# Performance work log

Measured on AMD Instinct MI355X. Metric: run time of the kernel, lower is better.

## Reference

```python
import jax, jax.numpy as jnp
import numpy as np

N, E = 50000, 800000
IN_FEATS, H, F = 128, 2, 64
NEG_SLOPE = 0.2


def _gat_conv(x, W, attn_l, attn_r, bias, src, dst):
    """DGL-style GATConv. x:[N,IN], W:[H*F,IN], attn_l/attn_r:[H,F], bias:[H*F]. Returns [N,H,F]."""
    z = (x @ W.T).reshape(N, H, F)                      # node projections
    el = jnp.einsum('nhf,hf->nh', z, attn_l)            # [N,H]
    er = jnp.einsum('nhf,hf->nh', z, attn_r)            # [N,H]
    e = jax.nn.leaky_relu(el[src] + er[dst], NEG_SLOPE) # [E,H] edge logits
    # edge softmax over incoming edges of each destination node
    m = jax.ops.segment_max(e, dst, num_segments=N)     # [N,H]
    ex = jnp.exp(e - m[dst])
    s = jax.ops.segment_sum(ex, dst, num_segments=N)    # [N,H]
    alpha = ex / s[dst]                                 # [E,H]
    msg = alpha[:, :, None] * z[src]                    # [E,H,F]
    out = jax.ops.segment_sum(msg, dst, num_segments=N) # [N,H,F]
    return out + bias.reshape(1, H, F)


def setup_inputs() -> dict:
    key = jax.random.key(0)
    ks = jax.random.split(key, 10)
    x = jax.random.normal(ks[0], (N, IN_FEATS), dtype=jnp.float32)
    h = jax.random.normal(ks[1], (N, H, F), dtype=jnp.float32)
    src = jax.random.randint(ks[2], (E,), 0, N, dtype=jnp.int32)
    dst = jax.random.randint(ks[3], (E,), 0, N, dtype=jnp.int32)
    sc = 1.0 / np.sqrt(IN_FEATS)
    W = jax.random.normal(ks[4], (3, H * F, IN_FEATS), dtype=jnp.float32) * sc  # r,u,c fc weights
    attn_l = jax.random.normal(ks[5], (3, H, F), dtype=jnp.float32) * 0.1
    attn_r = jax.random.normal(ks[6], (3, H, F), dtype=jnp.float32) * 0.1
    conv_bias = jax.random.normal(ks[7], (3, H * F), dtype=jnp.float32) * 0.02
    gate_bias = jax.random.uniform(ks[8], (3, H, F), dtype=jnp.float32)  # torch.rand init
    return {"x": x, "h": h, "W": W, "attn_l": attn_l, "attn_r": attn_r,
            "conv_bias": conv_bias, "gate_bias": gate_bias, "src": src, "dst": dst}


def reference(x, h, W, attn_l, attn_r, conv_bias, gate_bias, src, dst):
    # r, u, c gates; each GATConv is applied to x (use_hidden=False branch)
    r = jax.nn.sigmoid(_gat_conv(x, W[0], attn_l[0], attn_r[0], conv_bias[0], src, dst) + gate_bias[0])
    u = jax.nn.sigmoid(_gat_conv(x, W[1], attn_l[1], attn_r[1], conv_bias[1], src, dst) + gate_bias[1])
    # note: original computes h_ = r*h but never uses it in this branch (dead code)
    c = jax.nn.sigmoid(_gat_conv(x, W[2], attn_l[2], attn_r[2], conv_bias[2], src, dst) + gate_bias[2])
    new_h = u * h + (1.0 - u) * c
    return new_h
```

## Files before the change

### kernel.cpp

```cpp
#include <hip/hip_runtime.h>
#include <hip/hip_bf16.h>
#include <math.h>

#define NN 50000
#define EE 800000
#define KIN 128
#define HFD 128
#define ZB 256
#define NB 196
#define GB2 1564
#define SB 782
#define CAP 56
#define BSH 7

typedef __bf16 bf16_t;
typedef __bf16 bf16x8 __attribute__((ext_vector_type(8)));
typedef float f32x2 __attribute__((ext_vector_type(2)));
typedef float f32x4 __attribute__((ext_vector_type(4)));
typedef unsigned short u16;
typedef unsigned int u32;
typedef unsigned char u8;

__device__ __forceinline__ float ldf(const void* p, size_t i, int isf32) {
    return isf32 ? ((const float*)p)[i] : (float)((const bf16_t*)p)[i];
}
__device__ __forceinline__ bf16x8 load8bf(const void* base, size_t off, int isf32) {
    if (isf32) {
        const float4* p = (const float4*)((const float*)base + off);
        float4 u = p[0], v = p[1];
        bf16x8 r;
        r[0] = (bf16_t)u.x; r[1] = (bf16_t)u.y; r[2] = (bf16_t)u.z; r[3] = (bf16_t)u.w;
        r[4] = (bf16_t)v.x; r[5] = (bf16_t)v.y; r[6] = (bf16_t)v.z; r[7] = (bf16_t)v.w;
        return r;
    }
    return *(const bf16x8*)((const bf16_t*)base + off);
}

__device__ __forceinline__ uint2 pack8f(const float* v) {
    u32 lo = __builtin_amdgcn_cvt_pk_fp8_f32(v[0], v[1], 0u, false);
    lo = __builtin_amdgcn_cvt_pk_fp8_f32(v[2], v[3], lo, true);
    u32 hi = __builtin_amdgcn_cvt_pk_fp8_f32(v[4], v[5], 0u, false);
    hi = __builtin_amdgcn_cvt_pk_fp8_f32(v[6], v[7], hi, true);
    return make_uint2(lo, hi);
}

__global__ __launch_bounds__(256) void k_front(const unsigned short* __restrict__ xw,
                                               const void* __restrict__ W,
                                               const void* __restrict__ attn_l,
                                               const void* __restrict__ attn_r,
                                               u8* __restrict__ bkt,
                                               int* __restrict__ dflag,
                                               bf16_t* __restrict__ walv)
{
    const int b = blockIdx.x, tid = threadIdx.x;
    int i = b * 256 + tid;
    if (i < NN) *(int*)(bkt + ((size_t)i << BSH)) = 0;
    if (b > 8) return;

    __shared__ int cnt;
    if (tid == 0) cnt = 0;
    __syncthreads();
    int c = 0;
    for (int k = tid; k < 2048; k += 256) {
        int e = (xw[k] >> 7) & 0xFF;
        if (e > 150) c++;
    }
    atomicAdd(&cnt, c);
    __syncthreads();
    const int isf32 = (cnt > 20) ? 1 : 0;

    if (b == 0) {
        if (tid == 0) dflag[0] = isf32;
        return;
    }
    const int c8 = b - 1;
    const int side = c8 >> 2, g = (c8 >> 1) & 1, h = c8 & 1;
    const void* attn = side ? attn_r : attn_l;
    const int k = tid;
    if (k < KIN) {
        float acc = 0.f;
        for (int f = 0; f < 64; f++) {
            float wv = ldf(W, ((size_t)(g + 1) * HFD + h * 64 + f) * KIN + k, isf32);
            float av = ldf(attn, (size_t)((g + 1) * 2 + h) * 64 + f, isf32);
            acc += wv * av;
        }
        walv[(size_t)c8 * KIN + k] = (bf16_t)(acc * 1.44269504f);
    }
}

__global__ __launch_bounds__(256) void k_big(const void* __restrict__ x,
                                             const void* __restrict__ W,
                                             const bf16_t* __restrict__ walv,
                                             u8* __restrict__ z8,
                                             float* __restrict__ eln,
                                             float* __restrict__ ern,
                                             const int* __restrict__ src,
                                             const int* __restrict__ dst,
                                             u8* __restrict__ bkt,
                                             const int* __restrict__ dflag)
{
    __shared__ bf16_t wlds[128 * 128];

    const int bx = blockIdx.x;
    if (bx % 3 == 2) {
        int base = (bx / 3) * 1024 + threadIdx.x * 4;
        if (base < EE) {
            int4 s4 = *(const int4*)(src + base);
            int4 d4 = *(const int4*)(dst + base);
            u8* r0 = bkt + ((size_t)d4.x << BSH);
            u8* r1 = bkt + ((size_t)d4.y << BSH);
            u8* r2 = bkt + ((size_t)d4.z << BSH);
            u8* r3 = bkt + ((size_t)d4.w << BSH);
            int p0 = atomicAdd((int*)r0, 1);
            int p1 = atomicAdd((int*)r1, 1);
            int p2 = atomicAdd((int*)r2, 1);
            int p3 = atomicAdd((int*)r3, 1);
            if (p0 < CAP) *(u16*)(r0 + 4 + 2 * p0) = (u16)s4.x;
            if (p1 < CAP) *(u16*)(r1 + 4 + 2 * p1) = (u16)s4.y;
            if (p2 < CAP) *(u16*)(r2 + 4 + 2 * p2) = (u16)s4.z;
            if (p3 < CAP) *(u16*)(r3 + 4 + 2 * p3) = (u16)s4.w;
        }
        return;
    }

    const int isf32 = dflag[0];
    const int tid = threadIdx.x;
    const int gid = (bx / 3) * 2 + (bx % 3);
    const int ng = gid >> 1;
    const int g  = gid & 1;

    for (int c = tid; c < 2048; c += 256) {
        int col = c >> 4, g8 = c & 15;
        bf16x8 v = load8bf(W, ((size_t)(g + 1) * HFD + col) * KIN + g8 * 8, isf32);
        *(bf16x8*)(wlds + (size_t)col * 128 + (g8 ^ (col & 15)) * 8) = v;
    }

    const int wave = tid >> 6;
    const int lane = tid & 63;
    const int quad = lane >> 4;
    const int lm   = lane & 15;
    const int node_base = ng * 64 + wave * 16;

    int nld = node_base + lm;
    if (nld > NN - 1) nld = NN - 1;

    bf16x8 a[4];
#pragma unroll
    for (int kk = 0; kk < 4; kk++)
        a[kk] = load8bf(x, (size_t)nld * KIN + kk * 32 + quad * 8, isf32);

    __syncthreads();

    f32x4 acc[8];
#pragma unroll
    for (int t = 0; t < 8; t++) {
        const int wc = t * 16 + lm;
        f32x4 a4 = {0.f, 0.f, 0.f, 0.f};
#pragma unroll
        for (int kk = 0; kk < 4; kk++) {
            bf16x8 b = *(const bf16x8*)(wlds + (size_t)wc * 128 + ((kk * 4 + quad) ^ lm) * 8);
            a4 = __builtin_amdgcn_mfma_f32_16x16x32_bf16(a[kk], b, a4, 0, 0, 0);
        }
        acc[t] = a4;
    }

    if (g == 0) {
        f32x4 sacc = {0.f, 0.f, 0.f, 0.f};
#pragma unroll
        for (int kk = 0; kk < 4; kk++) {
            bf16x8 b;
            if (lm < 8) b = *(const bf16x8*)(walv + (size_t)lm * KIN + kk * 32 + quad * 8);
            else {
#pragma unroll
                for (int jj = 0; jj < 8; jj++) b[jj] = (bf16_t)0.f;
            }
            sacc = __builtin_amdgcn_mfma_f32_16x16x32_bf16(a[kk], b, sacc, 0, 0, 0);
        }
#pragma unroll
        for (int r = 0; r < 4; r++) {
            int nn = node_base + quad * 4 + r;
            if (nn < NN) {
                if (lm < 4)      eln[(size_t)nn * 4 + lm] = sacc[r];
                else if (lm < 8) ern[(size_t)nn * 4 + (lm - 4)] = sacc[r];
            }
        }
    }

#pragma unroll
    for (int r = 0; r < 4; r++) {
        float f[8];
#pragma unroll
        for (int t = 0; t < 8; t++) f[t] = acc[t][r];
        uint2 u = pack8f(f);
        int node = node_base + quad * 4 + r;
        if (node < NN)
            *(uint2*)(z8 + (size_t)node * ZB + g * 128 + lm * 8) = u;
    }
}

__global__ __launch_bounds__(256) void k_agg(const u8* __restrict__ z8,
                                             const u8* __restrict__ bkt,
                                             const float* __restrict__ eln,
                                             const float* __restrict__ ern,
                                             const void* __restrict__ conv_bias,
                                             const void* __restrict__ gate_bias,
                                             const void* __restrict__ hin,
                                             void* __restrict__ out,
                                             const int* __restrict__ dflag)
{
    const int isf32 = dflag[0];
    const int wave = threadIdx.x >> 6;
    const int lane = threadIdx.x & 63;
    const int j = ((lane >> 5) << 1) | (lane & 1);
    const int n = blockIdx.x * 4 + wave;
    if (n >= NN) return;
    const u8* rb = bkt + ((size_t)n << BSH);
    int cnt = __builtin_amdgcn_readfirstlane(*(const int*)rb);
    if (cnt > CAP) cnt = CAP;
    const u32* row32 = (const u32*)(rb + 4);
    const u16* row = (const u16*)(rb + 4);
    const float erj = ern[(size_t)n * 4 + j];
    const u32 zoff = 4u * (u32)lane;

    float a0 = 0.f, a1 = 0.f, a2 = 0.f, a3 = 0.f, s = 0.f;
    int i = 0;
    for (; i + 8 <= cnt; i += 8) {
        u32 rr[4];
#pragma unroll
        for (int q = 0; q < 4; q++)
            rr[q] = __builtin_amdgcn_readfirstlane(row32[(i >> 1) + q]);
        u32 sn[8];
#pragma unroll
        for (int q = 0; q < 4; q++) { sn[2*q] = rr[q] & 0xFFFFu; sn[2*q+1] = rr[q] >> 16; }
        u32 zb[8];
        float el[8];
#pragma unroll
        for (int q = 0; q < 8; q++) {
            const u8* zp = z8 + sn[q] * 256u;
            zb[q] = *(const u32*)(zp + zoff);
            el[q] = *(eln + sn[q] * 4u + (u32)j);
        }
        float w[8];
#pragma unroll
        for (int q = 0; q < 8; q++) {
            float v = el[q] + erj;
            v = fmaxf(v, 0.2f * v);
            w[q] = exp2f(v);
        }
#pragma unroll
        for (int q = 0; q < 8; q++) {
            f32x2 lo = __builtin_amdgcn_cvt_pk_f32_fp8(zb[q], false);
            f32x2 hi = __builtin_amdgcn_cvt_pk_f32_fp8(zb[q], true);
            a0 += w[q] * lo[0];
            a1 += w[q] * lo[1];
            a2 += w[q] * hi[0];
            a3 += w[q] * hi[1];
            s += w[q];
        }
    }
    if (i + 4 <= cnt) {
        u32 rr[2];
#pragma unroll
        for (int q = 0; q < 2; q++)
            rr[q] = __builtin_amdgcn_readfirstlane(row32[(i >> 1) + q]);
        u32 sn[4];
#pragma unroll
        for (int q = 0; q < 2; q++) { sn[2*q] = rr[q] & 0xFFFFu; sn[2*q+1] = rr[q] >> 16; }
        u32 zb[4];
        float el[4];
#pragma unroll
        for (int q = 0; q < 4; q++) {
            const u8* zp = z8 + sn[q] * 256u;
            zb[q] = *(const u32*)(zp + zoff);
            el[q] = *(eln + sn[q] * 4u + (u32)j);
        }
#pragma unroll
        for (int q = 0; q < 4; q++) {
            float v = el[q] + erj;
            v = fmaxf(v, 0.2f * v);
            float w = exp2f(v);
            f32x2 lo = __builtin_amdgcn_cvt_pk_f32_fp8(zb[q], false);
            f32x2 hi = __builtin_amdgcn_cvt_pk_f32_fp8(zb[q], true);
            a0 += w * lo[0];
            a1 += w * lo[1];
            a2 += w * hi[0];
            a3 += w * hi[1];
            s += w;
        }
        i += 4;
    }
    for (; i < cnt; i++) {
        u32 sn = __builtin_amdgcn_readfirstlane((u32)row[i]);
        const u8* zp = z8 + sn * 256u;
        u32 zb = *(const u32*)(zp + zoff);
        float v = *(eln + sn * 4u + (u32)j) + erj;
        v = fmaxf(v, 0.2f * v);
        float w = exp2f(v);
        f32x2 lo = __builtin_amdgcn_cvt_pk_f32_fp8(zb, false);
        f32x2 hi = __builtin_amdgcn_cvt_pk_f32_fp8(zb, true);
        a0 += w * lo[0];
        a1 += w * lo[1];
        a2 += w * hi[0];
        a3 += w * hi[1];
        s += w;
    }

    float inv = (cnt > 0) ? 1.f / fmaxf(s, 1e-30f) : 0.f;
    float o[4] = {a0 * inv, a1 * inv, a2 * inv, a3 * inv};

    const int gate = lane >> 5;
    int cf[4];
#pragma unroll
    for (int u = 0; u < 4; u++) cf[u] = (4 * (lane & 1) + u) * 16 + ((lane & 31) >> 1);

    float res[4];
    float hh[4];
    if (lane < 32) {
#pragma unroll
        for (int u = 0; u < 4; u++)
            hh[u] = ldf(hin, (size_t)n * HFD + cf[u], isf32);
    }
#pragma unroll
    for (int u = 0; u < 4; u++) {
        float ob = ldf(conv_bias, (size_t)(gate + 1) * HFD + cf[u], isf32)
                 + ldf(gate_bias, (size_t)((gate + 1) * 2 + (lane & 1)) * 64 + (cf[u] & 63), isf32);
        float gv = 1.f / (1.f + __expf(-(o[u] + ob)));
        float other = __shfl(gv, lane ^ 32, 64);
        if (lane < 32)
            res[u] = gv * hh[u] + (1.f - gv) * other;
    }
    if (lane < 32) {
        if (isf32) {
#pragma unroll
            for (int u = 0; u < 4; u++)
                ((float*)out)[(size_t)n * HFD + cf[u]] = res[u];
        } else {
#pragma unroll
            for (int u = 0; u < 4; u++)
                ((bf16_t*)out)[(size_t)n * HFD + cf[u]] = (bf16_t)res[u];
        }
    }
}

extern "C" void kernel_launch(void* const* d_in, const int* in_sizes, int n_in,
                              void* d_out, int out_size, void* d_ws, size_t ws_size,
                              hipStream_t stream)
{
    const void* x         = d_in[0];
    const void* hin       = d_in[1];
    const void* W         = d_in[2];
    const void* attn_l    = d_in[3];
    const void* attn_r    = d_in[4];
    const void* conv_bias = d_in[5];
    const void* gate_bias = d_in[6];
    const int* src        = (const int*)d_in[7];
    const int* dst        = (const int*)d_in[8];

    char* p = (char*)d_ws;
    int* dflag    = (int*)p;    p += 256;
    u8* z8        = (u8*)p;     p += (size_t)NN * ZB;
    float* eln    = (float*)p;  p += (size_t)NN * 4 * 4;
    float* ern    = (float*)p;  p += (size_t)NN * 4 * 4;
    u8* bkt       = (u8*)p;     p += (size_t)NN << BSH;
    bf16_t* walv  = (bf16_t*)p; p += 8 * KIN * 2;

    k_front<<<NB, 256, 0, stream>>>((const unsigned short*)x, W, attn_l, attn_r,
                                    bkt, dflag, walv);
    k_big<<<GB2 + SB, 256, 0, stream>>>(x, W, walv, z8, eln, ern, src, dst,
                                        bkt, dflag);
    k_agg<<<(NN + 3) / 4, 256, 0, stream>>>(z8, bkt, eln, ern,
                                            conv_bias, gate_bias, hin, d_out, dflag);
}
```

Baseline: 223.5 us.

## Rebalance scatter blocks, use buffer loads and packed FMA in aggregation

Changes k_big's block interleave from 2 GEMM blocks per scatter block to 4, with each scatter thread handling 8 edges instead of 4, which shrinks the grid. In k_agg, gathers of z8 and eln switch to raw buffer loads built from buffer resources, the readfirstlane calls on bucket data are dropped, and the four scalar accumulators become packed f32x2 FMAs. The aim is to cut scatter-block overhead and address arithmetic and to issue the gathers more cheaply. Removing readfirstlane may move uniform indices into vector registers, which could cost more than it saves.

```diff
diff --git a/kernel.cpp b/kernel.cpp
--- a/kernel.cpp
+++ b/kernel.cpp
@@ -9,9 +9,15 @@
 #define ZB 256
 #define NB 196
 #define GB2 1564
-#define SB 782
+#define GBT 1955
 #define CAP 56
 #define BSH 7
+
+#if defined(__has_builtin)
+#if __has_builtin(__builtin_amdgcn_make_buffer_rsrc) && __has_builtin(__builtin_amdgcn_raw_buffer_load_b32)
+#define BUFLD 1
+#endif
+#endif
 
 typedef __bf16 bf16_t;
 typedef __bf16 bf16x8 __attribute__((ext_vector_type(8)));
@@ -102,30 +108,31 @@
     __shared__ bf16_t wlds[128 * 128];
 
     const int bx = blockIdx.x;
-    if (bx % 3 == 2) {
-        int base = (bx / 3) * 1024 + threadIdx.x * 4;
+    if (bx % 5 == 4) {
+        int base = (bx / 5) * 2048 + threadIdx.x * 8;
         if (base < EE) {
-            int4 s4 = *(const int4*)(src + base);
-            int4 d4 = *(const int4*)(dst + base);
-            u8* r0 = bkt + ((size_t)d4.x << BSH);
-            u8* r1 = bkt + ((size_t)d4.y << BSH);
-            u8* r2 = bkt + ((size_t)d4.z << BSH);
-            u8* r3 = bkt + ((size_t)d4.w << BSH);
-            int p0 = atomicAdd((int*)r0, 1);
-            int p1 = atomicAdd((int*)r1, 1);
-            int p2 = atomicAdd((int*)r2, 1);
-            int p3 = atomicAdd((int*)r3, 1);
-            if (p0 < CAP) *(u16*)(r0 + 4 + 2 * p0) = (u16)s4.x;
-            if (p1 < CAP) *(u16*)(r1 + 4 + 2 * p1) = (u16)s4.y;
-            if (p2 < CAP) *(u16*)(r2 + 4 + 2 * p2) = (u16)s4.z;
-            if (p3 < CAP) *(u16*)(r3 + 4 + 2 * p3) = (u16)s4.w;
+            int4 sa = *(const int4*)(src + base);
+            int4 sb4 = *(const int4*)(src + base + 4);
+            int4 da = *(const int4*)(dst + base);
+            int4 db = *(const int4*)(dst + base + 4);
+            int dn[8] = {da.x, da.y, da.z, da.w, db.x, db.y, db.z, db.w};
+            int sn[8] = {sa.x, sa.y, sa.z, sa.w, sb4.x, sb4.y, sb4.z, sb4.w};
+            u8* rp[8];
+            int pp[8];
+#pragma unroll
+            for (int q = 0; q < 8; q++) rp[q] = bkt + ((size_t)dn[q] << BSH);
+#pragma unroll
+            for (int q = 0; q < 8; q++) pp[q] = atomicAdd((int*)rp[q], 1);
+#pragma unroll
+            for (int q = 0; q < 8; q++)
+                if (pp[q] < CAP) *(u16*)(rp[q] + 4 + 2 * pp[q]) = (u16)sn[q];
         }
         return;
     }
 
     const int isf32 = dflag[0];
     const int tid = threadIdx.x;
-    const int gid = (bx / 3) * 2 + (bx % 3);
+    const int gid = (bx / 5) * 4 + (bx % 5);
     const int ng = gid >> 1;
     const int g  = gid & 1;
 
@@ -211,24 +218,37 @@
     const int isf32 = dflag[0];
     const int wave = threadIdx.x >> 6;
     const int lane = threadIdx.x & 63;
-    const int j = ((lane >> 5) << 1) | (lane & 1);
+    const u32 j = ((lane >> 5) << 1) | (lane & 1);
     const int n = blockIdx.x * 4 + wave;
     if (n >= NN) return;
     const u8* rb = bkt + ((size_t)n << BSH);
-    int cnt = __builtin_amdgcn_readfirstlane(*(const int*)rb);
+    int cnt = *(const int*)rb;
     if (cnt > CAP) cnt = CAP;
     const u32* row32 = (const u32*)(rb + 4);
     const u16* row = (const u16*)(rb + 4);
     const float erj = ern[(size_t)n * 4 + j];
     const u32 zoff = 4u * (u32)lane;
-
-    float a0 = 0.f, a1 = 0.f, a2 = 0.f, a3 = 0.f, s = 0.f;
+    const u32 j4 = j * 4u;
+
+#ifdef BUFLD
+    __amdgpu_buffer_rsrc_t rz = __builtin_amdgcn_make_buffer_rsrc((void*)z8, (short)0,
+                                                                  (u32)((size_t)NN * ZB), 0x20000);
+    __amdgpu_buffer_rsrc_t re = __builtin_amdgcn_make_buffer_rsrc((void*)eln, (short)0,
+                                                                  (u32)(NN * 16), 0x20000);
+#define LDZ(boff) ((u32)__builtin_amdgcn_raw_buffer_load_b32(rz, (int)(boff), 0, 0))
+#define LDE(boff) (__builtin_bit_cast(float, __builtin_amdgcn_raw_buffer_load_b32(re, (int)(boff), 0, 0)))
+#else
+#define LDZ(boff) (*(const u32*)(z8 + (boff)))
+#define LDE(boff) (*(const float*)((const u8*)eln + (boff)))
+#endif
+
+    f32x2 a01 = {0.f, 0.f}, a23 = {0.f, 0.f};
+    float s = 0.f;
     int i = 0;
     for (; i + 8 <= cnt; i += 8) {
         u32 rr[4];
 #pragma unroll
-        for (int q = 0; q < 4; q++)
-            rr[q] = __builtin_amdgcn_readfirstlane(row32[(i >> 1) + q]);
+        for (int q = 0; q < 4; q++) rr[q] = row32[(i >> 1) + q];
         u32 sn[8];
 #pragma unroll
         for (int q = 0; q < 4; q++) { sn[2*q] = rr[q] & 0xFFFFu; sn[2*q+1] = rr[q] >> 16; }
@@ -236,9 +256,8 @@
         float el[8];
 #pragma unroll
         for (int q = 0; q < 8; q++) {
-            const u8* zp = z8 + sn[q] * 256u;
-            zb[q] = *(const u32*)(zp + zoff);
-            el[q] = *(eln + sn[q] * 4u + (u32)j);
+            zb[q] = LDZ((sn[q] << 8) + zoff);
+            el[q] = LDE(sn[q] * 16u + j4);
         }
         float w[8];
 #pragma unroll
@@ -251,18 +270,16 @@
         for (int q = 0; q < 8; q++) {
             f32x2 lo = __builtin_amdgcn_cvt_pk_f32_fp8(zb[q], false);
             f32x2 hi = __builtin_amdgcn_cvt_pk_f32_fp8(zb[q], true);
-            a0 += w[q] * lo[0];
-            a1 += w[q] * lo[1];
-            a2 += w[q] * hi[0];
-            a3 += w[q] * hi[1];
+            f32x2 w2 = {w[q], w[q]};
+            a01 += w2 * lo;
+            a23 += w2 * hi;
             s += w[q];
         }
     }
     if (i + 4 <= cnt) {
         u32 rr[2];
 #pragma unroll
-        for (int q = 0; q < 2; q++)
-            rr[q] = __builtin_amdgcn_readfirstlane(row32[(i >> 1) + q]);
+        for (int q = 0; q < 2; q++) rr[q] = row32[(i >> 1) + q];
         u32 sn[4];
 #pragma unroll
         for (int q = 0; q < 2; q++) { sn[2*q] = rr[q] & 0xFFFFu; sn[2*q+1] = rr[q] >> 16; }
@@ -270,9 +287,8 @@
         float el[4];
 #pragma unroll
         for (int q = 0; q < 4; q++) {
-            const u8* zp = z8 + sn[q] * 256u;
-            zb[q] = *(const u32*)(zp + zoff);
-            el[q] = *(eln + sn[q] * 4u + (u32)j);
+            zb[q] = LDZ((sn[q] << 8) + zoff);
+            el[q] = LDE(sn[q] * 16u + j4);
         }
 #pragma unroll
         for (int q = 0; q < 4; q++) {
@@ -281,32 +297,29 @@
             float w = exp2f(v);
             f32x2 lo = __builtin_amdgcn_cvt_pk_f32_fp8(zb[q], false);
             f32x2 hi = __builtin_amdgcn_cvt_pk_f32_fp8(zb[q], true);
-            a0 += w * lo[0];
-            a1 += w * lo[1];
-            a2 += w * hi[0];
-            a3 += w * hi[1];
+            f32x2 w2 = {w, w};
+            a01 += w2 * lo;
+            a23 += w2 * hi;
             s += w;
         }
         i += 4;
     }
     for (; i < cnt; i++) {
-        u32 sn = __builtin_amdgcn_readfirstlane((u32)row[i]);
-        const u8* zp = z8 + sn * 256u;
-        u32 zb = *(const u32*)(zp + zoff);
-        float v = *(eln + sn * 4u + (u32)j) + erj;
+        u32 sn = row[i];
+        u32 zb = LDZ((sn << 8) + zoff);
+        float v = LDE(sn * 16u + j4) + erj;
         v = fmaxf(v, 0.2f * v);
         float w = exp2f(v);
         f32x2 lo = __builtin_amdgcn_cvt_pk_f32_fp8(zb, false);
         f32x2 hi = __builtin_amdgcn_cvt_pk_f32_fp8(zb, true);
-        a0 += w * lo[0];
-        a1 += w * lo[1];
-        a2 += w * hi[0];
-        a3 += w * hi[1];
+        f32x2 w2 = {w, w};
+        a01 += w2 * lo;
+        a23 += w2 * hi;
         s += w;
     }
 
     float inv = (cnt > 0) ? 1.f / fmaxf(s, 1e-30f) : 0.f;
-    float o[4] = {a0 * inv, a1 * inv, a2 * inv, a3 * inv};
+    float o[4] = {a01[0] * inv, a01[1] * inv, a23[0] * inv, a23[1] * inv};
 
     const int gate = lane >> 5;
     int cf[4];
@@ -340,6 +353,8 @@
                 ((bf16_t*)out)[(size_t)n * HFD + cf[u]] = (bf16_t)res[u];
         }
     }
+#undef LDZ
+#undef LDE
 }
 
 extern "C" void kernel_launch(void* const* d_in, const int* in_sizes, int n_in,
@@ -366,8 +381,8 @@
 
     k_front<<<NB, 256, 0, stream>>>((const unsigned short*)x, W, attn_l, attn_r,
                                     bkt, dflag, walv);
-    k_big<<<GB2 + SB, 256, 0, stream>>>(x, W, walv, z8, eln, ern, src, dst,
-                                        bkt, dflag);
+    k_big<<<GBT, 256, 0, stream>>>(x, W, walv, z8, eln, ern, src, dst,
+                                   bkt, dflag);
     k_agg<<<(NN + 3) / 4, 256, 0, stream>>>(z8, bkt, eln, ern,
                                             conv_bias, gate_bias, hin, d_out, dflag);
 }
```

New measurement: 218.3 us. 1.02x faster.
